# Kernel optimization log

Hardware: AMD Instinct MI355X
Metric: run time of the kernel (lower is better)

Reference implementation:

```python
import jax, jax.numpy as jnp
import numpy as np
from jax import lax

V, D, B, L, T, H, C = 100000, 128, 512, 20, 20, 32, 33
N, E = B * L, B * (L - 1)
SCALE = 12.0

def _l2n(x, eps=1e-12):
    return x / (jnp.linalg.norm(x, axis=-1, keepdims=True) + eps)

def setup_inputs():
    key = jax.random.key(0)
    ks = jax.random.split(key, 30)
    stdv = 1.0 / np.sqrt(D)
    u = lambda k, s: jax.random.uniform(k, s, jnp.float32, -stdv, stdv)
    params = dict(
        emb=u(ks[0], (V, D)),
        W1=u(ks[1], (D, D)), W2=u(ks[2], (D, D)),
        gru_wih=u(ks[3], (3 * D, 2 * D)), gru_whh=u(ks[4], (3 * D, D)),
        gru_bih=u(ks[5], (3 * D,)), gru_bhh=u(ks[6], (3 * D,)),
        fcu_w=u(ks[7], (D, D)), fcv_w=u(ks[8], (D, D)), fcv_b=u(ks[9], (D,)),
        fce_w=u(ks[10], (D,)), fcsr_w=u(ks[11], (D, 2 * D)),
        red_w=u(ks[12], (H, D)), red_b=u(ks[13], (H,)),
        rec_w=u(ks[14], (D, H)), rec_b=u(ks[15], (D,)),
        cde_w1=u(ks[16], (128, H)), cde_b1=u(ks[17], (128,)),
        cde_w2=u(ks[18], (C * H, 128)), cde_b2=u(ks[19], (C * H,)),
        init_w=u(ks[20], (H, C)), init_b=u(ks[21], (H,)),
    )
    nodes = jnp.arange(N).reshape(B, L)  # B session graphs, L nodes each
    params.update(
        w=jax.random.uniform(ks[22], (E,), jnp.float32, 0.1, 1.0),
        times=jnp.cumsum(jax.random.uniform(ks[23], (B, T), jnp.float32, 0.05, 1.0), axis=1),
        iid=jax.random.randint(ks[24], (N,), 0, V),
        src=nodes[:, :-1].reshape(-1),
        dst=nodes[:, 1:].reshape(-1),
        seg_ids=jnp.repeat(jnp.arange(B), L),
        last_nodes=nodes[:, -1],
        embeds_ids=jax.random.randint(ks[25], (B, T), 0, V),
    )
    return params

def reference(emb, W1, W2, gru_wih, gru_whh, gru_bih, gru_bhh, fcu_w, fcv_w, fcv_b,
              fce_w, fcsr_w, red_w, red_b, rec_w, rec_b, cde_w1, cde_b1, cde_w2,
              cde_b2, init_w, init_b, w, times, iid, src, dst, seg_ids, last_nodes,
              embeds_ids):
    feat = _l2n(emb[iid])  # [N,D]
    # --- SRGNN layer: edge-weighted mean message passing (both directions) + GRUCell ---
    def wmean(s, d):
        msum = jax.ops.segment_sum(feat[s] * w[:, None], d, num_segments=N)
        wsum = jax.ops.segment_sum(w, d, num_segments=N)[:, None]
        return jnp.where(wsum > 0, msum / jnp.where(wsum == 0, 1.0, wsum), 0.0)
    hn = jnp.concatenate([wmean(src, dst) @ W1.T, wmean(dst, src) @ W2.T], axis=1)
    gi = hn @ gru_wih.T + gru_bih
    gh = feat @ gru_whh.T + gru_bhh
    i_r, i_z, i_n = jnp.split(gi, 3, axis=1)
    h_r, h_z, h_n = jnp.split(gh, 3, axis=1)
    r = jax.nn.sigmoid(i_r + h_r)
    zg = jax.nn.sigmoid(i_z + h_z)
    ng = jnp.tanh(i_n + r * h_n)
    out = (1.0 - zg) * ng + zg * feat  # NOTE: computed but unused downstream, exactly as original
    # --- neural CDE over the session item sequence (linear interp knots at t=0..T-1, RK4 per knot) ---
    fode = _l2n(emb[embeds_ids] @ red_w.T + red_b)          # [B,T,H]
    X = jnp.concatenate([times[..., None], fode], axis=-1)  # [B,T,C]
    z0 = X[:, 0] @ init_w.T + init_b                        # [B,H]
    def fz(zt):
        h1 = jax.nn.relu(zt @ cde_w1.T + cde_b1)
        return jnp.tanh(h1 @ cde_w2.T + cde_b2).reshape(B, H, C)
    dX = jnp.swapaxes(X[:, 1:] - X[:, :-1], 0, 1)           # [T-1,B,C] piecewise-constant dX/dt
    def step(zt, dx):
        g = lambda zz: jnp.einsum('bhc,bc->bh', fz(zz), dx)
        k1 = g(zt); k2 = g(zt + 0.5 * k1); k3 = g(zt + 0.5 * k2); k4 = g(zt + k3)
        return zt + (k1 + 2.0 * k2 + 2.0 * k3 + k4) / 6.0, None
    zT, _ = lax.scan(step, z0, dX)
    time_embeds = zT @ rec_w.T + rec_b                      # [B,D]
    # --- attention readout over graph segments ---
    featn = feat / jnp.linalg.norm(feat, axis=-1, keepdims=True)  # no-eps renorm, as original
    fu = featn @ fcu_w.T
    fv = featn[last_nodes] @ fcv_w.T + fcv_b
    e = jax.nn.sigmoid(fu + fv[seg_ids]) @ fce_w            # [N]
    emax = jax.ops.segment_max(e, seg_ids, num_segments=B)
    ee = jnp.exp(e - emax[seg_ids])
    alpha = ee / jax.ops.segment_sum(ee, seg_ids, num_segments=B)[seg_ids]
    sr_g = jax.ops.segment_sum(featn * alpha[:, None], seg_ids, num_segments=B)
    sr_l = featn[last_nodes]
    sr = _l2n(jnp.concatenate([sr_l, sr_g], axis=1) @ fcsr_w.T + time_embeds)
    logits = sr @ _l2n(emb).T                               # [B,V]
    return jax.nn.log_softmax(SCALE * logits, axis=-1)
```

## Files before the change

kernel.cpp:

```cpp
#include <hip/hip_runtime.h>
#include <cstdint>

#define VN 100000
#define DD 128
#define BB 512
#define LL 20
#define TT 20
#define HH 32
#define CC 33
#define NC (HH*CC)

typedef unsigned int u32;

#define DEV static __device__ __forceinline__

DEV float tanh_fast(float x){ float e=__expf(2.f*x); return 1.f - 2.f/(e+1.f); }

__global__ __launch_bounds__(256) void k_cde(
    const float* __restrict__ emb, const int* __restrict__ eids,
    const float* __restrict__ times,
    const float* __restrict__ red_w, const float* __restrict__ red_b,
    const float* __restrict__ w1, const float* __restrict__ b1,
    const float* __restrict__ w2, const float* __restrict__ b2,
    const float* __restrict__ iw, const float* __restrict__ ib,
    const float* __restrict__ rw, const float* __restrict__ rb,
    float* __restrict__ te){
  __shared__ float s_u[5120+4128];
  __shared__ float s_X[4*TT*CC];
  __shared__ float s_b1[DD];
  __shared__ float s_b2[NC];
  __shared__ float s_h1[4*DD];
  __shared__ float s_z[4*HH], s_zs[4*HH], s_ks[4*HH];
  __shared__ float s_dx[4*CC];
  float* s_er  = s_u;
  float* s_rw  = s_u + 5120;
  float* s_w1t = s_u;
  const int t = threadIdx.x;
  const int b0 = blockIdx.x*4;

  for(int i=t;i<HH*DD;i+=256){ int h=i>>7,d=i&127; s_rw[h*(DD+1)+d]=red_w[i]; }
  for(int i=t;i<DD;i+=256) s_b1[i]=b1[i];
  for(int i=t;i<NC;i+=256) s_b2[i]=b2[i];
  if(t<80){ int g=t/TT, tt2=t%TT;
    s_X[(g*TT+tt2)*CC]=times[(b0+g)*TT+tt2]; }
  for(int half=0; half<2; half++){
    __syncthreads();
    for(int p=t;p<40*DD;p+=256){
      int r=p>>7, e=p&127;
      s_er[p]=emb[(size_t)eids[b0*TT+half*40+r]*DD+e];
    }
    __syncthreads();
    for(int task=t; task<40*HH; task+=256){
      int r=task>>5, h=task&31;
      const float* wr=s_rw+h*(DD+1);
      const float* er=s_er+r*DD;
      float acc=red_b[h];
      #pragma unroll 16
      for(int e=0;e<DD;e++) acc += er[e]*wr[e];
      float s=acc*acc;
      #pragma unroll
      for(int o=16;o>0;o>>=1) s+=__shfl_xor(s,o,32);
      int rg=half*40+r;
      int g=rg/TT, tt2=rg%TT;
      s_X[(g*TT+tt2)*CC+1+h]=acc/(sqrtf(s)+1e-12f);
    }
  }
  __syncthreads();
  for(int i=t;i<HH*DD;i+=256){ int r=i>>5,h=i&31; s_w1t[h*DD+r]=w1[i]; }
  if(t<128){
    int g=t>>5, h=t&31;
    float acc=ib[h];
    const float* x0=s_X+(size_t)(g*TT)*CC;
    #pragma unroll
    for(int c=0;c<CC;c++) acc += x0[c]*iw[h*CC+c];
    s_z[g*HH+h]=acc; s_zs[g*HH+h]=acc;
  }
  const int h_b = t>>3;
  const int qc  = t&7;
  const int c0  = (qc==0)?0:(5+(qc-1)*4);
  const int ncr = (qc==0)?5:4;
  const int n0  = h_b*CC + c0;
  const float4* w2v=(const float4*)w2;

  for(int step=0; step<TT-1; step++){
    __syncthreads();
    if(t<4*CC){
      int g=t/CC, c=t-g*CC;
      s_dx[g*CC+c]=s_X[(g*TT+step+1)*CC+c]-s_X[(g*TT+step)*CC+c];
    }
    for(int s=0;s<4;s++){
      __syncthreads();
      {
        int g=t>>7, i=t&127;
        float a0=s_b1[i], a1=a0;
        #pragma unroll
        for(int h=0;h<HH;h++){
          float wv=s_w1t[h*DD+i];
          a0 += s_zs[g*HH+h]*wv;
          a1 += s_zs[(g+2)*HH+h]*wv;
        }
        s_h1[g*DD+i]=fmaxf(a0,0.f);
        s_h1[(g+2)*DD+i]=fmaxf(a1,0.f);
      }
      __syncthreads();
      float pk0=0.f,pk1=0.f,pk2=0.f,pk3=0.f;
      {
        float acc[5][4];
        #pragma unroll
        for(int r=0;r<5;r++){
          #pragma unroll
          for(int g=0;g<4;g++) acc[r][g]=0.f;
        }
        const float4* h4=(const float4*)s_h1;
        for(int j=0;j<16;j++){
          float hv[4][8];
          #pragma unroll
          for(int g=0;g<4;g++){
            float4 va=h4[g*32+j*2];
            float4 vb=h4[g*32+j*2+1];
            hv[g][0]=va.x; hv[g][1]=va.y; hv[g][2]=va.z; hv[g][3]=va.w;
            hv[g][4]=vb.x; hv[g][5]=vb.y; hv[g][6]=vb.z; hv[g][7]=vb.w;
          }
          #pragma unroll
          for(int r=0;r<5;r++){
            if(r<ncr){
              float4 ua=w2v[(size_t)(n0+r)*32+j*2];
              float4 ub=w2v[(size_t)(n0+r)*32+j*2+1];
              float wf[8];
              wf[0]=ua.x; wf[1]=ua.y; wf[2]=ua.z; wf[3]=ua.w;
              wf[4]=ub.x; wf[5]=ub.y; wf[6]=ub.z; wf[7]=ub.w;
              #pragma unroll
              for(int k=0;k<8;k++){
                float wk=wf[k];
                acc[r][0]+=wk*hv[0][k];
                acc[r][1]+=wk*hv[1][k];
                acc[r][2]+=wk*hv[2][k];
                acc[r][3]+=wk*hv[3][k];
              }
            }
          }
        }
        #pragma unroll
        for(int r=0;r<5;r++){
          if(r<ncr){
            int c=c0+r;
            float bb2=s_b2[n0+r];
            pk0 += tanh_fast(acc[r][0]+bb2)*s_dx[c];
            pk1 += tanh_fast(acc[r][1]+bb2)*s_dx[CC+c];
            pk2 += tanh_fast(acc[r][2]+bb2)*s_dx[2*CC+c];
            pk3 += tanh_fast(acc[r][3]+bb2)*s_dx[3*CC+c];
          }
        }
      }
      #pragma unroll
      for(int o=4;o>0;o>>=1){
        pk0 += __shfl_xor(pk0,o,8);
        pk1 += __shfl_xor(pk1,o,8);
        pk2 += __shfl_xor(pk2,o,8);
        pk3 += __shfl_xor(pk3,o,8);
      }
      if((t&7)==0){
        int h=t>>3;
        float pk[4]={pk0,pk1,pk2,pk3};
        #pragma unroll
        for(int g=0;g<4;g++){
          int idx=g*HH+h;
          float k=pk[g], zv=s_z[idx];
          if(s==0){ s_ks[idx]=k;        s_zs[idx]=zv+0.5f*k; }
          else if(s==1){ s_ks[idx]+=2.f*k; s_zs[idx]=zv+0.5f*k; }
          else if(s==2){ s_ks[idx]+=2.f*k; s_zs[idx]=zv+k; }
          else { float zn=zv+(s_ks[idx]+k)*(1.f/6.f); s_z[idx]=zn; s_zs[idx]=zn; }
        }
      }
    }
  }
  __syncthreads();
  {
    int g2=t>>7, d=t&127;
    #pragma unroll
    for(int gg=0; gg<2; gg++){
      int g=g2+2*gg;
      float acc=rb[d];
      #pragma unroll
      for(int h=0;h<HH;h++) acc += s_z[g*HH+h]*rw[d*HH+h];
      te[(size_t)(b0+g)*DD+d]=acc;
    }
  }
}

__global__ __launch_bounds__(128) void k_attn(
    const float* __restrict__ emb, const int* __restrict__ iid,
    const int* __restrict__ last_nodes,
    const float* __restrict__ fcu_w, const float* __restrict__ fcv_w,
    const float* __restrict__ fcv_b, const float* __restrict__ fce_w,
    const float* __restrict__ fcsr_w,
    const float* __restrict__ te, float* __restrict__ sr){
  __shared__ float s_fn[LL*DD];
  __shared__ float s_inv[LL];
  __shared__ float s_e[LL], s_alpha[LL], s_red[2], s_sg[DD], s_fl[DD];
  const int t=threadIdx.x, b=blockIdx.x;
  for(int p=t;p<LL*DD;p+=128){
    int r=p>>7, e=p&127;
    s_fn[p]=emb[(size_t)iid[b*LL+r]*DD+e];
  }
  __syncthreads();
  { int w=t>>6, lane=t&63;
    for(int r=w;r<LL;r+=2){
      float a=s_fn[r*DD+lane], c=s_fn[r*DD+lane+64];
      float s=a*a+c*c;
      #pragma unroll
      for(int o=32;o>0;o>>=1) s+=__shfl_xor(s,o,64);
      if(lane==0) s_inv[r]=1.f/sqrtf(s);
    }
  }
  __syncthreads();
  for(int p=t;p<LL*DD;p+=128) s_fn[p]*=s_inv[p>>7];
  __syncthreads();
  int lr=last_nodes[b]-b*LL; if(lr<0||lr>=LL) lr=LL-1;
  s_fl[t]=s_fn[lr*DD+t];
  __syncthreads();
  float fv;
  {
    float acc=fcv_b[t];
    const float* wv=fcv_w + t*DD;
    #pragma unroll 8
    for(int j=0;j<DD;j++) acc += s_fl[j]*wv[j];
    fv=acc;
  }
  const float fce=fce_w[t];
  const float* wu=fcu_w + t*DD;
  for(int n=0;n<LL;n++){
    float fu=0.f;
    #pragma unroll 8
    for(int j=0;j<DD;j++) fu += s_fn[n*DD+j]*wu[j];
    float sv = fce/(1.f+__expf(-(fu+fv)));
    #pragma unroll
    for(int o=32;o>0;o>>=1) sv += __shfl_xor(sv,o,64);
    if((t&63)==0) s_red[t>>6]=sv;
    __syncthreads();
    if(t==0) s_e[n]=s_red[0]+s_red[1];
    __syncthreads();
  }
  if(t<64){
    float ev=(t<LL)? s_e[t] : -1e30f;
    float m=ev;
    #pragma unroll
    for(int o=32;o>0;o>>=1) m=fmaxf(m,__shfl_xor(m,o,64));
    float ex=(t<LL)? __expf(ev-m):0.f;
    float ssum=ex;
    #pragma unroll
    for(int o=32;o>0;o>>=1) ssum+=__shfl_xor(ssum,o,64);
    if(t<LL) s_alpha[t]=ex/ssum;
  }
  __syncthreads();
  float sg=0.f;
  for(int n=0;n<LL;n++) sg += s_alpha[n]*s_fn[n*DD+t];
  s_sg[t]=sg;
  __syncthreads();
  float pre=te[(size_t)b*DD+t];
  const float* wsr=fcsr_w + t*2*DD;
  #pragma unroll 8
  for(int j=0;j<DD;j++) pre += s_fl[j]*wsr[j];
  #pragma unroll 8
  for(int j=0;j<DD;j++) pre += s_sg[j]*wsr[DD+j];
  float ss=pre*pre;
  #pragma unroll
  for(int o=32;o>0;o>>=1) ss+=__shfl_xor(ss,o,64);
  if((t&63)==0) s_red[t>>6]=ss;
  __syncthreads();
  float tot=s_red[0]+s_red[1];
  sr[(size_t)b*DD+t]=pre/(sqrtf(tot)+1e-12f);
}

__global__ __launch_bounds__(256) void k_logits(
    const float* __restrict__ emb, const float* __restrict__ srr,
    float* __restrict__ out){
  const int v=blockIdx.x*256+threadIdx.x;
  if(v>=VN) return;
  const int bstart=blockIdx.y*256;
  float er[DD];
  {
    const float4* ev=(const float4*)emb + (size_t)v*32;
    #pragma unroll
    for(int j=0;j<32;j++){
      float4 u=ev[j];
      er[j*4+0]=u.x; er[j*4+1]=u.y; er[j*4+2]=u.z; er[j*4+3]=u.w;
    }
  }
  float nrm=0.f;
  #pragma unroll
  for(int d=0;d<DD;d++) nrm += er[d]*er[d];
  const float rn=12.f/(sqrtf(nrm)+1e-12f);
  for(int b=bstart;b<bstart+256;b++){
    const float* s=srr+(size_t)b*DD;
    float acc=0.f;
    #pragma unroll
    for(int d=0;d<DD;d++) acc += er[d]*s[d];
    out[(size_t)b*VN+v]=acc*rn;
  }
}

__global__ __launch_bounds__(256) void k_lse(const float* __restrict__ out,
                                             float* __restrict__ lse){
  const int b=blockIdx.x, t=threadIdx.x;
  const float4* rp=(const float4*)(out + (size_t)b*VN);
  float m=-1e30f, s=0.f;
  for(int i=t;i<VN/4;i+=256){
    float4 x=rp[i];
    float mx=fmaxf(fmaxf(x.x,x.y),fmaxf(x.z,x.w));
    if(mx>m){ s=s*__expf(m-mx); m=mx; }
    s += __expf(x.x-m)+__expf(x.y-m)+__expf(x.z-m)+__expf(x.w-m);
  }
  __shared__ float sm[256], ssb[256];
  sm[t]=m; ssb[t]=s;
  __syncthreads();
  for(int o=128;o>0;o>>=1){
    if(t<o){
      float m1=sm[t], m2=sm[t+o], s1=ssb[t], s2=ssb[t+o];
      float mm=fmaxf(m1,m2);
      sm[t]=mm; ssb[t]=s1*__expf(m1-mm)+s2*__expf(m2-mm);
    }
    __syncthreads();
  }
  if(t==0) lse[b]=sm[0]+logf(ssb[0]);
}

__global__ __launch_bounds__(256) void k_sub(float* __restrict__ out,
                                             const float* __restrict__ lse){
  const size_t i=(size_t)blockIdx.x*256+threadIdx.x;
  const int b=(int)((i*4)/VN);
  const float l=lse[b];
  float4* p=(float4*)out;
  float4 x=p[i];
  x.x-=l; x.y-=l; x.z-=l; x.w-=l;
  p[i]=x;
}

extern "C" void kernel_launch(void* const* d_in, const int* in_sizes, int n_in,
                              void* d_out, int out_size, void* d_ws, size_t ws_size,
                              hipStream_t stream){
  const float* emb    = (const float*)d_in[0];
  const float* fcu_w  = (const float*)d_in[7];
  const float* fcv_w  = (const float*)d_in[8];
  const float* fcv_b  = (const float*)d_in[9];
  const float* fce_w  = (const float*)d_in[10];
  const float* fcsr_w = (const float*)d_in[11];
  const float* red_w  = (const float*)d_in[12];
  const float* red_b  = (const float*)d_in[13];
  const float* rec_w  = (const float*)d_in[14];
  const float* rec_b  = (const float*)d_in[15];
  const float* cde_w1 = (const float*)d_in[16];
  const float* cde_b1 = (const float*)d_in[17];
  const float* cde_w2 = (const float*)d_in[18];
  const float* cde_b2 = (const float*)d_in[19];
  const float* init_w = (const float*)d_in[20];
  const float* init_b = (const float*)d_in[21];
  const float* times  = (const float*)d_in[23];
  const int* iid    = (const int*)d_in[24];
  const int* last_nodes = (const int*)d_in[28];
  const int* embeds_ids = (const int*)d_in[29];
  float* out = (float*)d_out;

  float* ws  = (float*)d_ws;
  float* te  = ws;
  float* sr  = te + (size_t)BB*DD;
  float* lse = sr + (size_t)BB*DD;

  k_cde   <<<BB/4, 256, 0, stream>>>(emb, embeds_ids, times, red_w, red_b,
                                     cde_w1, cde_b1, cde_w2, cde_b2,
                                     init_w, init_b, rec_w, rec_b, te);
  k_attn  <<<BB, 128, 0, stream>>>(emb, iid, last_nodes, fcu_w, fcv_w, fcv_b,
                                   fce_w, fcsr_w, te, sr);
  k_logits<<<dim3((VN+255)/256, 2), 256, 0, stream>>>(emb, sr, out);
  k_lse   <<<BB, 256, 0, stream>>>(out, lse);
  k_sub   <<<(int)(((size_t)BB*VN/4+255)/256), 256, 0, stream>>>(out, lse);
}
```

Measured before the change: 3.232 ms.

## Keep CDE w2 weights register-resident and broadcast hidden state via readlane

The CDE kernel now processes 2 sessions per block with 576 threads. Each thread holds its rows of cde_w2 in registers for the whole RK4 integration instead of re-reading them from global memory at every stage. Hidden activations and z are broadcast across the wavefront with readlane, and one extra wave handles the 33rd channel column. This removes repeated global weight traffic in the serial ODE loop. The cost is very high register pressure (256 floats per thread) with possible spills, plus doubling the block count with fewer sessions per block.

```diff
diff --git a/kernel.cpp b/kernel.cpp
--- a/kernel.cpp
+++ b/kernel.cpp
@@ -16,7 +16,11 @@
 
 DEV float tanh_fast(float x){ float e=__expf(2.f*x); return 1.f - 2.f/(e+1.f); }
 
-__global__ __launch_bounds__(256) void k_cde(
+DEV float rdlane(float v, int l){
+  return __int_as_float(__builtin_amdgcn_readlane(__float_as_int(v), l));
+}
+
+__global__ __launch_bounds__(576) void k_cde(
     const float* __restrict__ emb, const int* __restrict__ eids,
     const float* __restrict__ times,
     const float* __restrict__ red_w, const float* __restrict__ red_b,
@@ -25,166 +29,162 @@
     const float* __restrict__ iw, const float* __restrict__ ib,
     const float* __restrict__ rw, const float* __restrict__ rb,
     float* __restrict__ te){
-  __shared__ float s_u[5120+4128];
-  __shared__ float s_X[4*TT*CC];
+  __shared__ float s_u[40*DD + 32*129];
+  __shared__ float s_X[2*TT*CC];
   __shared__ float s_b1[DD];
-  __shared__ float s_b2[NC];
-  __shared__ float s_h1[4*DD];
-  __shared__ float s_z[4*HH], s_zs[4*HH], s_ks[4*HH];
-  __shared__ float s_dx[4*CC];
-  float* s_er  = s_u;
-  float* s_rw  = s_u + 5120;
-  float* s_w1t = s_u;
+  __shared__ float s_h1[2*DD];
+  __shared__ float s_z[64], s_zs[64], s_ks[64], s_kp[64], s_kt[64];
+  __shared__ float s_dx[2*CC];
   const int t = threadIdx.x;
-  const int b0 = blockIdx.x*4;
-
-  for(int i=t;i<HH*DD;i+=256){ int h=i>>7,d=i&127; s_rw[h*(DD+1)+d]=red_w[i]; }
-  for(int i=t;i<DD;i+=256) s_b1[i]=b1[i];
-  for(int i=t;i<NC;i+=256) s_b2[i]=b2[i];
-  if(t<80){ int g=t/TT, tt2=t%TT;
-    s_X[(g*TT+tt2)*CC]=times[(b0+g)*TT+tt2]; }
-  for(int half=0; half<2; half++){
-    __syncthreads();
-    for(int p=t;p<40*DD;p+=256){
-      int r=p>>7, e=p&127;
-      s_er[p]=emb[(size_t)eids[b0*TT+half*40+r]*DD+e];
-    }
-    __syncthreads();
-    for(int task=t; task<40*HH; task+=256){
-      int r=task>>5, h=task&31;
-      const float* wr=s_rw+h*(DD+1);
-      const float* er=s_er+r*DD;
-      float acc=red_b[h];
-      #pragma unroll 16
-      for(int e=0;e<DD;e++) acc += er[e]*wr[e];
-      float s=acc*acc;
-      #pragma unroll
-      for(int o=16;o>0;o>>=1) s+=__shfl_xor(s,o,32);
-      int rg=half*40+r;
-      int g=rg/TT, tt2=rg%TT;
-      s_X[(g*TT+tt2)*CC+1+h]=acc/(sqrtf(s)+1e-12f);
-    }
-  }
-  __syncthreads();
-  for(int i=t;i<HH*DD;i+=256){ int r=i>>5,h=i&31; s_w1t[h*DD+r]=w1[i]; }
-  if(t<128){
-    int g=t>>5, h=t&31;
-    float acc=ib[h];
+  const int b0 = blockIdx.x*2;
+  const int lane = t & 63;
+  float* s_er = s_u;
+  float* s_rw = s_u + 40*DD;
+  float* s_w1 = s_u;
+
+  float w2a[DD], w2b[DD];
+  float b2a, b2b;
+  int hq=0, qq=0;
+  if (t < 512){
+    hq = t>>4; qq = t&15;
+    const int n0 = hq*CC + 2*qq;
+    const float4* r0=(const float4*)(w2+(size_t)n0*DD);
+    const float4* r1=(const float4*)(w2+(size_t)(n0+1)*DD);
+    #pragma unroll 32
+    for(int j=0;j<32;j++){
+      float4 a=r0[j];
+      w2a[4*j]=a.x; w2a[4*j+1]=a.y; w2a[4*j+2]=a.z; w2a[4*j+3]=a.w;
+    }
+    #pragma unroll 32
+    for(int j=0;j<32;j++){
+      float4 bv=r1[j];
+      w2b[4*j]=bv.x; w2b[4*j+1]=bv.y; w2b[4*j+2]=bv.z; w2b[4*j+3]=bv.w;
+    }
+    b2a=b2[n0]; b2b=b2[n0+1];
+  } else {
+    const int l=t-512; const int nt=(l&31)*CC+32;
+    const float4* r0=(const float4*)(w2+(size_t)nt*DD);
+    #pragma unroll 32
+    for(int j=0;j<32;j++){
+      float4 a=r0[j];
+      w2a[4*j]=a.x; w2a[4*j+1]=a.y; w2a[4*j+2]=a.z; w2a[4*j+3]=a.w;
+    }
+    b2a=b2[nt]; b2b=0.f;
+  }
+
+  for (int i=t;i<HH*DD;i+=576){ int hh=i>>7, d=i&127; s_rw[hh*129+d]=red_w[i]; }
+  if (t<40){ int g=t/TT, tt2=t%TT; s_X[(g*TT+tt2)*CC]=times[(b0+g)*TT+tt2]; }
+  for (int p=t;p<40*DD;p+=576){ int r=p>>7, e=p&127;
+      s_er[p]=emb[(size_t)eids[b0*TT + r]*DD + e]; }
+  __syncthreads();
+  for (int task=t; task<40*HH; task+=576){
+    int r=task>>5, hh=task&31;
+    const float* wr=s_rw+hh*129;
+    const float* er=s_er+(size_t)r*DD;
+    float acc=red_b[hh];
+    #pragma unroll 16
+    for(int e=0;e<DD;e++) acc += er[e]*wr[e];
+    float ss=acc*acc;
+    #pragma unroll
+    for(int o=16;o>0;o>>=1) ss+=__shfl_xor(ss,o,32);
+    s_X[r*CC+1+hh]=acc/(sqrtf(ss)+1e-12f);
+  }
+  __syncthreads();
+  for (int i=t;i<DD*HH;i+=576){ int j=i>>5, hh=i&31; s_w1[j*33+hh]=w1[i]; }
+  if (t<DD) s_b1[t]=b1[t];
+  if (t<64){
+    int g=t>>5, hh=t&31;
+    float acc=ib[hh];
     const float* x0=s_X+(size_t)(g*TT)*CC;
     #pragma unroll
-    for(int c=0;c<CC;c++) acc += x0[c]*iw[h*CC+c];
-    s_z[g*HH+h]=acc; s_zs[g*HH+h]=acc;
-  }
-  const int h_b = t>>3;
-  const int qc  = t&7;
-  const int c0  = (qc==0)?0:(5+(qc-1)*4);
-  const int ncr = (qc==0)?5:4;
-  const int n0  = h_b*CC + c0;
-  const float4* w2v=(const float4*)w2;
-
-  for(int step=0; step<TT-1; step++){
-    __syncthreads();
-    if(t<4*CC){
-      int g=t/CC, c=t-g*CC;
-      s_dx[g*CC+c]=s_X[(g*TT+step+1)*CC+c]-s_X[(g*TT+step)*CC+c];
-    }
-    for(int s=0;s<4;s++){
-      __syncthreads();
-      {
-        int g=t>>7, i=t&127;
-        float a0=s_b1[i], a1=a0;
-        #pragma unroll
-        for(int h=0;h<HH;h++){
-          float wv=s_w1t[h*DD+i];
-          a0 += s_zs[g*HH+h]*wv;
-          a1 += s_zs[(g+2)*HH+h]*wv;
-        }
-        s_h1[g*DD+i]=fmaxf(a0,0.f);
-        s_h1[(g+2)*DD+i]=fmaxf(a1,0.f);
+    for(int c=0;c<CC;c++) acc += x0[c]*iw[hh*CC+c];
+    s_z[t]=acc; s_zs[t]=acc;
+  }
+
+  for (int step=0; step<TT-1; step++){
+    __syncthreads();
+    if (t<2*CC){ int g=t/CC, c=t-g*CC;
+      s_dx[t]=s_X[(g*TT+step+1)*CC+c]-s_X[(g*TT+step)*CC+c]; }
+    __syncthreads();
+    float dx00=0.f,dx01=0.f,dx10=0.f,dx11=0.f,dxt=0.f;
+    if (t<512){ int c0=2*qq;
+      dx00=s_dx[c0]; dx01=s_dx[c0+1]; dx10=s_dx[CC+c0]; dx11=s_dx[CC+c0+1];
+    } else { int l=t-512; dxt=s_dx[(l>>5)*CC+32]; }
+
+    for (int s=0;s<4;s++){
+      if (t<256){
+        const int g=t>>7, j=t&127, gb=(t>>7)*32;
+        float zsv=s_zs[lane];
+        float acc=s_b1[j];
+        const float* wj=s_w1+j*33;
+        #pragma unroll 32
+        for(int hh=0;hh<32;hh++) acc += rdlane(zsv, gb+hh)*wj[hh];
+        s_h1[g*DD+j]=fmaxf(acc,0.f);
       }
       __syncthreads();
-      float pk0=0.f,pk1=0.f,pk2=0.f,pk3=0.f;
-      {
-        float acc[5][4];
+      float h00=s_h1[lane],    h01=s_h1[64+lane];
+      float h10=s_h1[DD+lane], h11=s_h1[DD+64+lane];
+      if (t<512){
+        float a00=b2a, a10=b2b, a01=b2a, a11=b2b;
+        #pragma unroll 64
+        for(int j=0;j<64;j++){
+          float s0=rdlane(h00,j), s1=rdlane(h10,j);
+          a00+=s0*w2a[j]; a10+=s0*w2b[j];
+          a01+=s1*w2a[j]; a11+=s1*w2b[j];
+        }
+        #pragma unroll 64
+        for(int j=0;j<64;j++){
+          float s0=rdlane(h01,j), s1=rdlane(h11,j);
+          a00+=s0*w2a[64+j]; a10+=s0*w2b[64+j];
+          a01+=s1*w2a[64+j]; a11+=s1*w2b[64+j];
+        }
+        float pk0=tanh_fast(a00)*dx00 + tanh_fast(a10)*dx01;
+        float pk1=tanh_fast(a01)*dx10 + tanh_fast(a11)*dx11;
         #pragma unroll
-        for(int r=0;r<5;r++){
-          #pragma unroll
-          for(int g=0;g<4;g++) acc[r][g]=0.f;
-        }
-        const float4* h4=(const float4*)s_h1;
-        for(int j=0;j<16;j++){
-          float hv[4][8];
-          #pragma unroll
-          for(int g=0;g<4;g++){
-            float4 va=h4[g*32+j*2];
-            float4 vb=h4[g*32+j*2+1];
-            hv[g][0]=va.x; hv[g][1]=va.y; hv[g][2]=va.z; hv[g][3]=va.w;
-            hv[g][4]=vb.x; hv[g][5]=vb.y; hv[g][6]=vb.z; hv[g][7]=vb.w;
-          }
-          #pragma unroll
-          for(int r=0;r<5;r++){
-            if(r<ncr){
-              float4 ua=w2v[(size_t)(n0+r)*32+j*2];
-              float4 ub=w2v[(size_t)(n0+r)*32+j*2+1];
-              float wf[8];
-              wf[0]=ua.x; wf[1]=ua.y; wf[2]=ua.z; wf[3]=ua.w;
-              wf[4]=ub.x; wf[5]=ub.y; wf[6]=ub.z; wf[7]=ub.w;
-              #pragma unroll
-              for(int k=0;k<8;k++){
-                float wk=wf[k];
-                acc[r][0]+=wk*hv[0][k];
-                acc[r][1]+=wk*hv[1][k];
-                acc[r][2]+=wk*hv[2][k];
-                acc[r][3]+=wk*hv[3][k];
-              }
-            }
-          }
-        }
-        #pragma unroll
-        for(int r=0;r<5;r++){
-          if(r<ncr){
-            int c=c0+r;
-            float bb2=s_b2[n0+r];
-            pk0 += tanh_fast(acc[r][0]+bb2)*s_dx[c];
-            pk1 += tanh_fast(acc[r][1]+bb2)*s_dx[CC+c];
-            pk2 += tanh_fast(acc[r][2]+bb2)*s_dx[2*CC+c];
-            pk3 += tanh_fast(acc[r][3]+bb2)*s_dx[3*CC+c];
-          }
-        }
+        for(int o=8;o>0;o>>=1){
+          pk0+=__shfl_xor(pk0,o,16);
+          pk1+=__shfl_xor(pk1,o,16);
+        }
+        if (qq==0){ s_kp[hq]=pk0; s_kp[32+hq]=pk1; }
+      } else {
+        const int l=t-512, gq=l>>5, ht=l&31;
+        float a0=0.f, a1=0.f;
+        #pragma unroll 64
+        for(int j=0;j<64;j++){
+          a0+=rdlane(h00,j)*w2a[j];
+          a1+=rdlane(h10,j)*w2a[j];
+        }
+        #pragma unroll 64
+        for(int j=0;j<64;j++){
+          a0+=rdlane(h01,j)*w2a[64+j];
+          a1+=rdlane(h11,j)*w2a[64+j];
+        }
+        float av = b2a + (gq ? a1 : a0);
+        s_kt[gq*32+ht]=tanh_fast(av)*dxt;
       }
-      #pragma unroll
-      for(int o=4;o>0;o>>=1){
-        pk0 += __shfl_xor(pk0,o,8);
-        pk1 += __shfl_xor(pk1,o,8);
-        pk2 += __shfl_xor(pk2,o,8);
-        pk3 += __shfl_xor(pk3,o,8);
+      __syncthreads();
+      if (t<64){
+        float k=s_kp[t]+s_kt[t];
+        float zv=s_z[t];
+        if(s==0){ s_ks[t]=k;        s_zs[t]=zv+0.5f*k; }
+        else if(s==1){ s_ks[t]+=2.f*k; s_zs[t]=zv+0.5f*k; }
+        else if(s==2){ s_ks[t]+=2.f*k; s_zs[t]=zv+k; }
+        else { float zn=zv+(s_ks[t]+k)*(1.f/6.f); s_z[t]=zn; s_zs[t]=zn; }
       }
-      if((t&7)==0){
-        int h=t>>3;
-        float pk[4]={pk0,pk1,pk2,pk3};
-        #pragma unroll
-        for(int g=0;g<4;g++){
-          int idx=g*HH+h;
-          float k=pk[g], zv=s_z[idx];
-          if(s==0){ s_ks[idx]=k;        s_zs[idx]=zv+0.5f*k; }
-          else if(s==1){ s_ks[idx]+=2.f*k; s_zs[idx]=zv+0.5f*k; }
-          else if(s==2){ s_ks[idx]+=2.f*k; s_zs[idx]=zv+k; }
-          else { float zn=zv+(s_ks[idx]+k)*(1.f/6.f); s_z[idx]=zn; s_zs[idx]=zn; }
-        }
-      }
-    }
-  }
-  __syncthreads();
-  {
-    int g2=t>>7, d=t&127;
-    #pragma unroll
-    for(int gg=0; gg<2; gg++){
-      int g=g2+2*gg;
-      float acc=rb[d];
-      #pragma unroll
-      for(int h=0;h<HH;h++) acc += s_z[g*HH+h]*rw[d*HH+h];
-      te[(size_t)(b0+g)*DD+d]=acc;
-    }
+      __syncthreads();
+    }
+  }
+  if (t<256){
+    const int g=t>>7, d=t&127;
+    float acc=rb[d];
+    const float* zz=s_z+g*HH;
+    const float4* rv=(const float4*)(rw + (size_t)d*HH);
+    #pragma unroll 8
+    for(int jj=0;jj<8;jj++){
+      float4 vv=rv[jj];
+      acc += zz[4*jj]*vv.x + zz[4*jj+1]*vv.y + zz[4*jj+2]*vv.z + zz[4*jj+3]*vv.w;
+    }
+    te[(size_t)(b0+g)*DD+d]=acc;
   }
 }
 
@@ -366,7 +366,7 @@
   float* sr  = te + (size_t)BB*DD;
   float* lse = sr + (size_t)BB*DD;
 
-  k_cde   <<<BB/4, 256, 0, stream>>>(emb, embeds_ids, times, red_w, red_b,
+  k_cde   <<<BB/2, 576, 0, stream>>>(emb, embeds_ids, times, red_w, red_b,
                                      cde_w1, cde_b1, cde_w2, cde_b2,
                                      init_w, init_b, rec_w, rec_b, te);
   k_attn  <<<BB, 128, 0, stream>>>(emb, iid, last_nodes, fcu_w, fcv_w, fcv_b,
```

Measured after the change: 2.831 ms. 1.14x faster.
